# Kernel optimization log

Measured on AMD Instinct MI355X. Metric: run time of the kernel, lower is better.

## Reference

```python
import jax, jax.numpy as jnp
import numpy as np

EPS = 1e-10

def _cc_module(q, k, v):
    # q,k: [Bp, Cq, h, w]; v: [Bp, C, h, w]
    # cosine-normalize over channel dim (matches torch dim=-1 on (b,h,c) / dim=1 on (b,c,h))
    qn = q / (jnp.sqrt(jnp.sum(q * q, axis=1, keepdims=True)) + EPS)
    kn = k / (jnp.sqrt(jnp.sum(k * k, axis=1, keepdims=True)) + EPS)
    h = q.shape[2]
    energy_H = jnp.einsum('bchw,bcgw->bhwg', qn, kn)  # keys along column (height)
    energy_W = jnp.einsum('bchw,bchg->bhwg', qn, kn)  # keys along row (width)
    att = jax.nn.softmax(jnp.concatenate([energy_H, energy_W], axis=-1), axis=-1)
    att_H, att_W = att[..., :h], att[..., h:]
    out_H = jnp.einsum('bcgw,bhwg->bchw', v, att_H)
    out_W = jnp.einsum('bchg,bhwg->bchw', v, att_W)
    return out_H + out_W

def _grid_pa(q, k, v, nbin):
    # batch all bin*bin local patches of the grid into the leading dim
    B, C, H, W = v.shape
    ph, pw = H // nbin, W // nbin
    def split(t):
        c = t.shape[1]
        return t.reshape(B, c, nbin, ph, nbin, pw).transpose(0, 2, 4, 1, 3, 5).reshape(B * nbin * nbin, c, ph, pw)
    out = _cc_module(split(q), split(k), split(v))
    return out.reshape(B, nbin, nbin, C, ph, pw).transpose(0, 3, 1, 4, 2, 5).reshape(B, C, H, W)

def _conv1x1(x, w, b):
    return jnp.einsum('bchw,oc->bohw', x, w) + b[None, :, None, None]

def _cam(x, gamma):
    # channel attention: cosine similarity between channel vectors over spatial dim
    B, C, H, W = x.shape
    f = x.reshape(B, C, H * W)
    a = f / (jnp.sqrt(jnp.sum(f * f, axis=-1, keepdims=True)) + EPS)
    energy = jnp.einsum('bin,bjn->bij', a, a)  # [B, C, C]
    att = jax.nn.softmax(energy, axis=-1)
    out = jnp.einsum('bij,bjn->bin', att, f).reshape(B, C, H, W)
    return gamma * out + x

def setup_inputs() -> dict:
    key = jax.random.key(0)
    ks = jax.random.split(key, 8)
    B, C, H, W = 4, 512, 128, 128
    Cq = C // 4
    s = 0.05
    return {
        'x': jax.random.normal(ks[0], (B, C, H, W), jnp.float32),
        'w_q': jax.random.normal(ks[1], (Cq, C), jnp.float32) * s,
        'b_q': jnp.zeros((Cq,), jnp.float32),
        'w_k': jax.random.normal(ks[2], (Cq, C), jnp.float32) * s,
        'b_k': jnp.zeros((Cq,), jnp.float32),
        'w_v': jax.random.normal(ks[3], (C, C), jnp.float32) * s,
        'b_v': jnp.zeros((C,), jnp.float32),
        'gamma': jax.random.normal(ks[4], (1,), jnp.float32) * 0.1,
        'nbin': 4,
    }

def reference(x, w_q, b_q, w_k, b_k, w_v, b_v, gamma, nbin):
    # mode 'p_c_s': two rounds of grid criss-cross attention, then channel attention
    for _ in range(2):
        q = _conv1x1(x, w_q, b_q)
        k = _conv1x1(x, w_k, b_k)
        v = _conv1x1(x, w_v, b_v)
        x = _grid_pa(q, k, v, nbin)
    return _cam(x, gamma)
```

## Files before the change

kernel.cpp:

```cpp
#include <hip/hip_runtime.h>
#include <math.h>

constexpr int Bn = 4;
constexpr int Cc = 512;
constexpr int CQ = 128;
constexpr int Hh = 128, Ww = 128;
constexpr int Nn = Hh * Ww;
constexpr int NPATCH = 64;
constexpr float EPSf = 1e-10f;

typedef unsigned int u32;
typedef unsigned short u16;
typedef __attribute__((ext_vector_type(8))) short bf16x8;
typedef __attribute__((ext_vector_type(4))) float f32x4;

__device__ inline u16 f2bf(float f) {
    u32 u = __float_as_uint(f);
    u32 r = u + 0x7fffu + ((u >> 16) & 1u);
    return (u16)(r >> 16);
}
__device__ inline float bf2f(u16 h) { return __uint_as_float((u32)h << 16); }

#define GLOAD16(g, l) __builtin_amdgcn_global_load_lds( \
    (const __attribute__((address_space(1))) u32*)(g), \
    (__attribute__((address_space(3))) u32*)(l), 16, 0, 0)


__global__ __launch_bounds__(256) void conv_w(
    const float* __restrict__ wq, const float* __restrict__ bq,
    const float* __restrict__ wk, const float* __restrict__ bk,
    const float* __restrict__ wv, const float* __restrict__ bv,
    u16* __restrict__ wh, u16* __restrict__ wl, float* __restrict__ bcat)
{
    const int oc = blockIdx.x;
    const float* src; float bias;
    if (oc < 128)      { src = wq + (size_t)oc * 512;        bias = bq[oc]; }
    else if (oc < 256) { src = wk + (size_t)(oc-128) * 512;  bias = bk[oc-128]; }
    else               { src = wv + (size_t)(oc-256) * 512;  bias = bv[oc-256]; }
    for (int c = threadIdx.x; c < 512; c += 256) {
        float v = src[c];
        u16 h = f2bf(v);
        wh[(size_t)oc*512 + c] = h;
        wl[(size_t)oc*512 + c] = f2bf(v - bf2f(h));
    }
    if (threadIdx.x == 0) bcat[oc] = bias;
}

__global__ __launch_bounds__(256) void conv_x_t(
    const float* __restrict__ x, u16* __restrict__ xh, u16* __restrict__ xl)
{
    __shared__ float T[64][65];
    const int n0 = blockIdx.x * 64, c0 = blockIdx.y * 64, b = blockIdx.z;
    const int t = threadIdx.x;
    {
        const int cc = t >> 2, nn = (t & 3) * 16;
        const float* s = x + ((size_t)b*Cc + c0 + cc)*Nn + n0 + nn;
        #pragma unroll
        for (int u = 0; u < 16; u += 4) {
            float4 v = *(const float4*)(s + u);
            T[cc][nn+u]=v.x; T[cc][nn+u+1]=v.y; T[cc][nn+u+2]=v.z; T[cc][nn+u+3]=v.w;
        }
    }
    __syncthreads();
    {
        const int nn = t >> 2, cc0 = (t & 3) * 16;
        u16 hs[16] __attribute__((aligned(16)));
        u16 ls[16] __attribute__((aligned(16)));
        #pragma unroll
        for (int e = 0; e < 16; e++) {
            float v = T[cc0+e][nn];
            u16 h = f2bf(v);
            hs[e] = h; ls[e] = f2bf(v - bf2f(h));
        }
        const size_t o = ((size_t)b*Nn + n0 + nn)*Cc + c0 + cc0;
        *(uint4*)&xh[o]   = *(const uint4*)&hs[0];
        *(uint4*)&xh[o+8] = *(const uint4*)&hs[8];
        *(uint4*)&xl[o]   = *(const uint4*)&ls[0];
        *(uint4*)&xl[o+8] = *(const uint4*)&ls[8];
    }
}

__global__ __launch_bounds__(256) void conv_cl(
    const float* __restrict__ s, u16* __restrict__ h, u16* __restrict__ l, long n)
{
    const long i = (((long)blockIdx.x << 8) + threadIdx.x) << 3;
    if (i >= n) return;
    float4 a = *(const float4*)(s + i), b4 = *(const float4*)(s + i + 4);
    float v[8] = {a.x,a.y,a.z,a.w,b4.x,b4.y,b4.z,b4.w};
    u16 hs[8] __attribute__((aligned(16)));
    u16 ls[8] __attribute__((aligned(16)));
    #pragma unroll
    for (int e = 0; e < 8; e++) {
        u16 hh = f2bf(v[e]);
        hs[e] = hh; ls[e] = f2bf(v[e] - bf2f(hh));
    }
    *(uint4*)&h[i] = *(const uint4*)hs;
    *(uint4*)&l[i] = *(const uint4*)ls;
}

__global__ __launch_bounds__(256) void conv_t_cl(
    const float* __restrict__ x1, u16* __restrict__ th, u16* __restrict__ tl)
{
    __shared__ float T[64][65];
    const int n0 = blockIdx.x * 64, c0 = blockIdx.y * 64, b = blockIdx.z;
    const int t = threadIdx.x;
    {
        const int nn = t >> 2, cc0 = (t & 3) * 16;
        const float* s = x1 + ((size_t)b*Nn + n0 + nn)*Cc + c0 + cc0;
        #pragma unroll
        for (int u = 0; u < 16; u += 4) {
            float4 v = *(const float4*)(s + u);
            T[nn][cc0+u]=v.x; T[nn][cc0+u+1]=v.y; T[nn][cc0+u+2]=v.z; T[nn][cc0+u+3]=v.w;
        }
    }
    __syncthreads();
    {
        const int cc = t >> 2, nn0 = (t & 3) * 16;
        u16 hs[16] __attribute__((aligned(16)));
        u16 ls[16] __attribute__((aligned(16)));
        #pragma unroll
        for (int e = 0; e < 16; e++) {
            float v = T[nn0+e][cc];
            u16 h = f2bf(v);
            hs[e] = h; ls[e] = f2bf(v - bf2f(h));
        }
        const size_t o = ((size_t)b*Cc + c0 + cc)*Nn + n0 + nn0;
        *(uint4*)&th[o]   = *(const uint4*)&hs[0];
        *(uint4*)&th[o+8] = *(const uint4*)&hs[8];
        *(uint4*)&tl[o]   = *(const uint4*)&ls[0];
        *(uint4*)&tl[o+8] = *(const uint4*)&ls[8];
    }
}


__global__ __launch_bounds__(256) void qkv_mfma(
    const u16* __restrict__ xh, const u16* __restrict__ xl,
    const u16* __restrict__ wh, const u16* __restrict__ wl,
    const float* __restrict__ bcat,
    float* __restrict__ q_t, float* __restrict__ k_t, float* __restrict__ v_t)
{
    __shared__ char Ash[16384];
    __shared__ char Bsh[16384];
    const int t = threadIdx.x, lane = t & 63, wid = t >> 6;
    const int n0 = blockIdx.x * 128, oc0 = blockIdx.y * 128, b = blockIdx.z;
    const size_t bN = (size_t)b * Nn;

    float* outp; int ocb, OC;
    if (oc0 == 0)        { outp = q_t; ocb = 0;         OC = CQ; }
    else if (oc0 == 128) { outp = k_t; ocb = 0;         OC = CQ; }
    else                 { outp = v_t; ocb = oc0 - 256; OC = Cc; }

    const u16* sA[4]; const u16* sB[4];
    #pragma unroll
    for (int q = 0; q < 4; q++) {
        const int p = ((wid*4 + q) << 10) + lane*16;
        const int row = p >> 7;
        const int lchunk = ((p >> 4) & 7) ^ (row & 7);
        const int ko = (lchunk & 3) * 8;
        sA[q] = ((lchunk < 4) ? xh : xl) + (bN + n0 + row)*(size_t)Cc + ko;
        sB[q] = ((lchunk < 4) ? wh : wl) + (size_t)(oc0 + row)*Cc + ko;
    }

    const int wr = wid >> 1, wc = wid & 1;
    int aoff[4], boff[4];
    #pragma unroll
    for (int m = 0; m < 4; m++) {
        const int ra = (wr << 6) + (m << 4) + (lane & 15);
        aoff[m] = (ra << 7) + ((((lane >> 4) << 4)) ^ ((ra & 7) << 4));
        const int rb = (wc << 6) + (m << 4) + (lane & 15);
        boff[m] = (rb << 7) + ((((lane >> 4) << 4)) ^ ((rb & 7) << 4));
    }

    f32x4 acc[4][4];
    #pragma unroll
    for (int m = 0; m < 4; m++)
        #pragma unroll
        for (int n = 0; n < 4; n++) acc[m][n] = (f32x4){0.f, 0.f, 0.f, 0.f};

    for (int ks = 0; ks < 16; ks++) {
        if (ks) __syncthreads();
        #pragma unroll
        for (int q = 0; q < 4; q++) {
            GLOAD16(sA[q], Ash + ((wid*4 + q) << 10));
            GLOAD16(sB[q], Bsh + ((wid*4 + q) << 10));
            sA[q] += 32; sB[q] += 32;
        }
        __syncthreads();
        bf16x8 ah[4], al[4], bh[4], bl[4];
        #pragma unroll
        for (int m = 0; m < 4; m++) {
            ah[m] = *(const bf16x8*)(Ash + aoff[m]);
            al[m] = *(const bf16x8*)(Ash + (aoff[m] ^ 64));
            bh[m] = *(const bf16x8*)(Bsh + boff[m]);
            bl[m] = *(const bf16x8*)(Bsh + (boff[m] ^ 64));
        }
        #pragma unroll
        for (int m = 0; m < 4; m++)
            #pragma unroll
            for (int n = 0; n < 4; n++) {
                acc[m][n] = __builtin_amdgcn_mfma_f32_16x16x32_bf16(ah[m], bh[n], acc[m][n], 0, 0, 0);
                acc[m][n] = __builtin_amdgcn_mfma_f32_16x16x32_bf16(ah[m], bl[n], acc[m][n], 0, 0, 0);
                acc[m][n] = __builtin_amdgcn_mfma_f32_16x16x32_bf16(al[m], bh[n], acc[m][n], 0, 0, 0);
            }
    }

    const int col = lane & 15, rq = lane >> 4;
    #pragma unroll
    for (int n = 0; n < 4; n++) {
        const int oc = (wc << 6) + (n << 4) + col;
        const float bias = bcat[oc0 + oc];
        #pragma unroll
        for (int m = 0; m < 4; m++) {
            #pragma unroll
            for (int r = 0; r < 4; r++) {
                const int nrow = n0 + (wr << 6) + (m << 4) + (rq << 2) + r;
                outp[(bN + nrow)*OC + ocb + oc] = acc[m][n][r] + bias;
            }
        }
    }
}

__global__ __launch_bounds__(256) void gram_mfma(
    const u16* __restrict__ fTh, const u16* __restrict__ fTl,
    float* __restrict__ Gp)
{
    __shared__ char Ash[16384];
    __shared__ char Bsh[16384];
    const int t = threadIdx.x, lane = t & 63, wid = t >> 6;
    const int i0 = blockIdx.x * 128, j0 = blockIdx.y * 128;
    const int b = blockIdx.z >> 3, kc = blockIdx.z & 7;
    const size_t cb = (size_t)b * 512 * Nn;

    const u16* sA[4]; const u16* sB[4];
    #pragma unroll
    for (int q = 0; q < 4; q++) {
        const int p = ((wid*4 + q) << 10) + lane*16;
        const int row = p >> 7;
        const int lchunk = ((p >> 4) & 7) ^ (row & 7);
        const int ko = (lchunk & 3) * 8;
        const u16* s = (lchunk < 4) ? fTh : fTl;
        sA[q] = s + cb + (size_t)(i0 + row)*Nn + kc*2048 + ko;
        sB[q] = s + cb + (size_t)(j0 + row)*Nn + kc*2048 + ko;
    }

    const int wr = wid >> 1, wc = wid & 1;
    int aoff[4], boff[4];
    #pragma unroll
    for (int m = 0; m < 4; m++) {
        const int ra = (wr << 6) + (m << 4) + (lane & 15);
        aoff[m] = (ra << 7) + ((((lane >> 4) << 4)) ^ ((ra & 7) << 4));
        const int rb = (wc << 6) + (m << 4) + (lane & 15);
        boff[m] = (rb << 7) + ((((lane >> 4) << 4)) ^ ((rb & 7) << 4));
    }

    f32x4 acc[4][4];
    #pragma unroll
    for (int m = 0; m < 4; m++)
        #pragma unroll
        for (int n = 0; n < 4; n++) acc[m][n] = (f32x4){0.f, 0.f, 0.f, 0.f};

    for (int ks = 0; ks < 64; ks++) {
        if (ks) __syncthreads();
        #pragma unroll
        for (int q = 0; q < 4; q++) {
            GLOAD16(sA[q], Ash + ((wid*4 + q) << 10));
            GLOAD16(sB[q], Bsh + ((wid*4 + q) << 10));
            sA[q] += 32; sB[q] += 32;
        }
        __syncthreads();
        bf16x8 ah[4], al[4], bh[4], bl[4];
        #pragma unroll
        for (int m = 0; m < 4; m++) {
            ah[m] = *(const bf16x8*)(Ash + aoff[m]);
            al[m] = *(const bf16x8*)(Ash + (aoff[m] ^ 64));
            bh[m] = *(const bf16x8*)(Bsh + boff[m]);
            bl[m] = *(const bf16x8*)(Bsh + (boff[m] ^ 64));
        }
        #pragma unroll
        for (int m = 0; m < 4; m++)
            #pragma unroll
            for (int n = 0; n < 4; n++) {
                acc[m][n] = __builtin_amdgcn_mfma_f32_16x16x32_bf16(ah[m], bh[n], acc[m][n], 0, 0, 0);
                acc[m][n] = __builtin_amdgcn_mfma_f32_16x16x32_bf16(ah[m], bl[n], acc[m][n], 0, 0, 0);
                acc[m][n] = __builtin_amdgcn_mfma_f32_16x16x32_bf16(al[m], bh[n], acc[m][n], 0, 0, 0);
            }
    }

    float* gp = Gp + (size_t)(kc*4 + b) * 512 * 512;
    const int col = lane & 15, rq = lane >> 4;
    #pragma unroll
    for (int m = 0; m < 4; m++)
        #pragma unroll
        for (int r = 0; r < 4; r++) {
            const int ri = i0 + (wr << 6) + (m << 4) + (rq << 2) + r;
            #pragma unroll
            for (int n = 0; n < 4; n++)
                gp[(size_t)ri*512 + j0 + (wc << 6) + (n << 4) + col] = acc[m][n][r];
        }
}

__global__ __launch_bounds__(256) void camout_mfma(
    const u16* __restrict__ Ph, const u16* __restrict__ Pl,
    const u16* __restrict__ x1h, const u16* __restrict__ x1l,
    const u16* __restrict__ fTh, const u16* __restrict__ fTl,
    const float* __restrict__ gamma, float* __restrict__ out)
{
    __shared__ char Ash[16384];
    __shared__ char Bsh[16384];
    const int t = threadIdx.x, lane = t & 63, wid = t >> 6;
    const int n0 = blockIdx.x * 128, i0 = blockIdx.y * 128, b = blockIdx.z;
    const size_t bN = (size_t)b * Nn;

    const u16* sA[4]; const u16* sB[4];
    #pragma unroll
    for (int q = 0; q < 4; q++) {
        const int p = ((wid*4 + q) << 10) + lane*16;
        const int row = p >> 7;
        const int lchunk = ((p >> 4) & 7) ^ (row & 7);
        const int ko = (lchunk & 3) * 8;
        sA[q] = ((lchunk < 4) ? Ph : Pl) + ((size_t)b*512 + i0 + row)*512 + ko;
        sB[q] = ((lchunk < 4) ? x1h : x1l) + (bN + n0 + row)*(size_t)Cc + ko;
    }

    const int wr = wid >> 1, wc = wid & 1;
    int aoff[4], boff[4];
    #pragma unroll
    for (int m = 0; m < 4; m++) {
        const int ra = (wr << 6) + (m << 4) + (lane & 15);
        aoff[m] = (ra << 7) + ((((lane >> 4) << 4)) ^ ((ra & 7) << 4));
        const int rb = (wc << 6) + (m << 4) + (lane & 15);
        boff[m] = (rb << 7) + ((((lane >> 4) << 4)) ^ ((rb & 7) << 4));
    }

    f32x4 acc[4][4];
    #pragma unroll
    for (int m = 0; m < 4; m++)
        #pragma unroll
        for (int n = 0; n < 4; n++) acc[m][n] = (f32x4){0.f, 0.f, 0.f, 0.f};

    for (int ks = 0; ks < 16; ks++) {
        if (ks) __syncthreads();
        #pragma unroll
        for (int q = 0; q < 4; q++) {
            GLOAD16(sA[q], Ash + ((wid*4 + q) << 10));
            GLOAD16(sB[q], Bsh + ((wid*4 + q) << 10));
            sA[q] += 32; sB[q] += 32;
        }
        __syncthreads();
        bf16x8 ah[4], al[4], bh[4], bl[4];
        #pragma unroll
        for (int m = 0; m < 4; m++) {
            ah[m] = *(const bf16x8*)(Ash + aoff[m]);
            al[m] = *(const bf16x8*)(Ash + (aoff[m] ^ 64));
            bh[m] = *(const bf16x8*)(Bsh + boff[m]);
            bl[m] = *(const bf16x8*)(Bsh + (boff[m] ^ 64));
        }
        #pragma unroll
        for (int m = 0; m < 4; m++)
            #pragma unroll
            for (int n = 0; n < 4; n++) {
                acc[m][n] = __builtin_amdgcn_mfma_f32_16x16x32_bf16(ah[m], bh[n], acc[m][n], 0, 0, 0);
                acc[m][n] = __builtin_amdgcn_mfma_f32_16x16x32_bf16(ah[m], bl[n], acc[m][n], 0, 0, 0);
                acc[m][n] = __builtin_amdgcn_mfma_f32_16x16x32_bf16(al[m], bh[n], acc[m][n], 0, 0, 0);
            }
    }

    const float gm = gamma[0];
    const int col = lane & 15, rq = lane >> 4;
    #pragma unroll
    for (int m = 0; m < 4; m++)
        #pragma unroll
        for (int r = 0; r < 4; r++) {
            const int i = i0 + (wr << 6) + (m << 4) + (rq << 2) + r;
            const size_t rb = ((size_t)b*512 + i)*Nn;
            #pragma unroll
            for (int n = 0; n < 4; n++) {
                const int nn = n0 + (wc << 6) + (n << 4) + col;
                const float res = bf2f(fTh[rb + nn]) + bf2f(fTl[rb + nn]);
                out[rb + nn] = fmaf(gm, acc[m][n][r], res);
            }
        }
}

__global__ __launch_bounds__(256) void qk_norms(
    const float* __restrict__ q_t, const float* __restrict__ k_t,
    float* __restrict__ nq, float* __restrict__ nk)
{
    const int pos = blockIdx.x * 256 + threadIdx.x;
    const float* qp = q_t + (size_t)pos * CQ;
    const float* kp = k_t + (size_t)pos * CQ;
    float sq = 0.f, sk = 0.f;
    #pragma unroll
    for (int c = 0; c < CQ; c += 4) {
        float4 a = *(const float4*)&qp[c];
        float4 bb = *(const float4*)&kp[c];
        sq += a.x*a.x + a.y*a.y + a.z*a.z + a.w*a.w;
        sk += bb.x*bb.x + bb.y*bb.y + bb.z*bb.z + bb.w*bb.w;
    }
    nq[pos] = sqrtf(sq) + EPSf;
    nk[pos] = sqrtf(sk) + EPSf;
}

__global__ __launch_bounds__(256) void energy_H(
    const float* __restrict__ q_t, const float* __restrict__ k_t,
    const float* __restrict__ nq, const float* __restrict__ nk,
    float* __restrict__ att)
{
    __shared__ float Qs[32][129], Ks[32][129];
    __shared__ float nqs[32], nks[32];
    const int w = blockIdx.x, p = blockIdx.y;
    const int b = p >> 4, pi = (p >> 2) & 3, pj = p & 3;
    const int gw = pj*32 + w;
    const int t = threadIdx.x;
    {
        const int h  = t >> 3;
        const int c0 = (t & 7) * 16;
        const size_t base = ((size_t)b*Nn + (size_t)(pi*32 + h)*Ww + gw) * CQ + c0;
        #pragma unroll
        for (int u = 0; u < 16; u += 4) {
            float4 qa = *(const float4*)&q_t[base + u];
            float4 ka = *(const float4*)&k_t[base + u];
            Qs[h][c0+u]=qa.x; Qs[h][c0+u+1]=qa.y; Qs[h][c0+u+2]=qa.z; Qs[h][c0+u+3]=qa.w;
            Ks[h][c0+u]=ka.x; Ks[h][c0+u+1]=ka.y; Ks[h][c0+u+2]=ka.z; Ks[h][c0+u+3]=ka.w;
        }
    }
    if (t < 32) {
        const size_t pp = (size_t)b*Nn + (size_t)(pi*32 + t)*Ww + gw;
        nqs[t] = nq[pp]; nks[t] = nk[pp];
    }
    __syncthreads();
    const int h0 = (t & 15) * 2, g0 = (t >> 4) * 2;
    float a00=0,a01=0,a10=0,a11=0;
    #pragma unroll 4
    for (int c = 0; c < CQ; c++) {
        float q0 = Qs[h0][c], q1 = Qs[h0+1][c];
        float k0 = Ks[g0][c], k1 = Ks[g0+1][c];
        a00 = fmaf(q0,k0,a00); a01 = fmaf(q0,k1,a01);
        a10 = fmaf(q1,k0,a10); a11 = fmaf(q1,k1,a11);
    }
    const size_t ab = (((size_t)p*32 + h0)*32 + w)*64;
    att[ab + g0]            = a00 / (nqs[h0]   * nks[g0]);
    att[ab + g0 + 1]        = a01 / (nqs[h0]   * nks[g0+1]);
    att[ab + 2048 + g0]     = a10 / (nqs[h0+1] * nks[g0]);
    att[ab + 2048 + g0 + 1] = a11 / (nqs[h0+1] * nks[g0+1]);
}

__global__ __launch_bounds__(256) void energy_W(
    const float* __restrict__ q_t, const float* __restrict__ k_t,
    const float* __restrict__ nq, const float* __restrict__ nk,
    float* __restrict__ att)
{
    __shared__ float Qs[32][129], Ks[32][129];
    __shared__ float nqs[32], nks[32];
    const int h = blockIdx.x, p = blockIdx.y;
    const int b = p >> 4, pi = (p >> 2) & 3, pj = p & 3;
    const int gh = pi*32 + h;
    const size_t rowpos = (size_t)b*Nn + (size_t)gh*Ww + pj*32;
    const int t = threadIdx.x;
    {
        const int wl = t >> 3;
        const int c0 = (t & 7) * 16;
        const size_t base = (rowpos + wl) * CQ + c0;
        #pragma unroll
        for (int u = 0; u < 16; u += 4) {
            float4 qa = *(const float4*)&q_t[base + u];
            float4 ka = *(const float4*)&k_t[base + u];
            Qs[wl][c0+u]=qa.x; Qs[wl][c0+u+1]=qa.y; Qs[wl][c0+u+2]=qa.z; Qs[wl][c0+u+3]=qa.w;
            Ks[wl][c0+u]=ka.x; Ks[wl][c0+u+1]=ka.y; Ks[wl][c0+u+2]=ka.z; Ks[wl][c0+u+3]=ka.w;
        }
    }
    if (t < 32) { nqs[t] = nq[rowpos + t]; nks[t] = nk[rowpos + t]; }
    __syncthreads();
    const int w0 = (t & 15) * 2, g0 = (t >> 4) * 2;
    float a00=0,a01=0,a10=0,a11=0;
    #pragma unroll 4
    for (int c = 0; c < CQ; c++) {
        float q0 = Qs[w0][c], q1 = Qs[w0+1][c];
        float k0 = Ks[g0][c], k1 = Ks[g0+1][c];
        a00 = fmaf(q0,k0,a00); a01 = fmaf(q0,k1,a01);
        a10 = fmaf(q1,k0,a10); a11 = fmaf(q1,k1,a11);
    }
    const size_t ab = (((size_t)p*32 + h)*32 + w0)*64 + 32;
    att[ab + g0]          = a00 / (nqs[w0]   * nks[g0]);
    att[ab + g0 + 1]      = a01 / (nqs[w0]   * nks[g0+1]);
    att[ab + 64 + g0]     = a10 / (nqs[w0+1] * nks[g0]);
    att[ab + 64 + g0 + 1] = a11 / (nqs[w0+1] * nks[g0+1]);
}

__global__ __launch_bounds__(256) void softmax64(float* __restrict__ att)
{
    const size_t idx = (size_t)blockIdx.x * 256 + threadIdx.x;
    float* row = att + idx * 64;
    float v[64];
    float m = -1e30f;
    #pragma unroll
    for (int i = 0; i < 64; i += 4) {
        float4 x4 = *(const float4*)&row[i];
        v[i]=x4.x; v[i+1]=x4.y; v[i+2]=x4.z; v[i+3]=x4.w;
        m = fmaxf(m, fmaxf(fmaxf(x4.x,x4.y), fmaxf(x4.z,x4.w)));
    }
    float s = 0.f;
    #pragma unroll
    for (int i = 0; i < 64; i++) { v[i] = __expf(v[i] - m); s += v[i]; }
    const float inv = 1.f / s;
    #pragma unroll
    for (int i = 0; i < 64; i += 4) {
        float4 x4 = {v[i]*inv, v[i+1]*inv, v[i+2]*inv, v[i+3]*inv};
        *(float4*)&row[i] = x4;
    }
}

__global__ __launch_bounds__(256) void cc_outH(
    const float* __restrict__ v_t, const float* __restrict__ att,
    float* __restrict__ x1)
{
    __shared__ float Vs[32][256];
    __shared__ float At[32][33];
    const int w = blockIdx.x, p = blockIdx.y;
    const int b = p >> 4, pi = (p >> 2) & 3, pj = p & 3;
    const int gw = pj*32 + w;
    const int t = threadIdx.x;
    {
        const int hh = t >> 3, g0 = (t & 7) * 4;
        const float* arow = att + (((size_t)p*32 + hh)*32 + w)*64 + g0;
        float4 a = *(const float4*)arow;
        At[g0][hh]=a.x; At[g0+1][hh]=a.y; At[g0+2][hh]=a.z; At[g0+3][hh]=a.w;
    }
    const int s  = t & 63, hg = t >> 6;
    const int cl = s * 4, h0 = hg * 8;
    for (int half = 0; half < 2; half++) {
        __syncthreads();
        {
            const int g = t >> 3, c0 = (t & 7) * 32;
            const float* src = v_t + ((size_t)b*Nn + (size_t)(pi*32 + g)*Ww + gw)*Cc + half*256 + c0;
            #pragma unroll
            for (int u = 0; u < 32; u += 4)
                *(float4*)&Vs[g][c0+u] = *(const float4*)&src[u];
        }
        __syncthreads();
        float acc[8][4];
        #pragma unroll
        for (int i = 0; i < 8; i++) { acc[i][0]=0.f; acc[i][1]=0.f; acc[i][2]=0.f; acc[i][3]=0.f; }
        #pragma unroll 4
        for (int g = 0; g < 32; g++) {
            const float4 va = *(const float4*)&Vs[g][cl];
            #pragma unroll
            for (int hh = 0; hh < 8; hh++) {
                const float a = At[g][h0+hh];
                acc[hh][0] = fmaf(va.x, a, acc[hh][0]);
                acc[hh][1] = fmaf(va.y, a, acc[hh][1]);
                acc[hh][2] = fmaf(va.z, a, acc[hh][2]);
                acc[hh][3] = fmaf(va.w, a, acc[hh][3]);
            }
        }
        #pragma unroll
        for (int hh = 0; hh < 8; hh++) {
            float4 o = {acc[hh][0], acc[hh][1], acc[hh][2], acc[hh][3]};
            *(float4*)&x1[((size_t)b*Nn + (size_t)(pi*32 + h0+hh)*Ww + gw)*Cc + half*256 + cl] = o;
        }
    }
}

__global__ __launch_bounds__(256) void cc_outW(
    const float* __restrict__ v_t, const float* __restrict__ att,
    float* __restrict__ x1)
{
    __shared__ float Vs[32][256];
    __shared__ float At[32][33];
    const int h = blockIdx.x, p = blockIdx.y;
    const int b = p >> 4, pi = (p >> 2) & 3, pj = p & 3;
    const int gh = pi*32 + h;
    const size_t rowpos = (size_t)b*Nn + (size_t)gh*Ww + pj*32;
    const int t = threadIdx.x;
    {
        const int wl = t >> 3, g0 = (t & 7) * 4;
        const float* arow = att + (((size_t)p*32 + h)*32 + wl)*64 + 32 + g0;
        float4 a = *(const float4*)arow;
        At[g0][wl]=a.x; At[g0+1][wl]=a.y; At[g0+2][wl]=a.z; At[g0+3][wl]=a.w;
    }
    const int s  = t & 63, wg = t >> 6;
    const int cl = s * 4, w0 = wg * 8;
    for (int half = 0; half < 2; half++) {
        __syncthreads();
        {
            const int g = t >> 3, c0 = (t & 7) * 32;
            const float* src = v_t + (rowpos + g)*Cc + half*256 + c0;
            #pragma unroll
            for (int u = 0; u < 32; u += 4)
                *(float4*)&Vs[g][c0+u] = *(const float4*)&src[u];
        }
        __syncthreads();
        float acc[8][4];
        #pragma unroll
        for (int i = 0; i < 8; i++) { acc[i][0]=0.f; acc[i][1]=0.f; acc[i][2]=0.f; acc[i][3]=0.f; }
        #pragma unroll 4
        for (int g = 0; g < 32; g++) {
            const float4 va = *(const float4*)&Vs[g][cl];
            #pragma unroll
            for (int ww = 0; ww < 8; ww++) {
                const float a = At[g][w0+ww];
                acc[ww][0] = fmaf(va.x, a, acc[ww][0]);
                acc[ww][1] = fmaf(va.y, a, acc[ww][1]);
                acc[ww][2] = fmaf(va.z, a, acc[ww][2]);
                acc[ww][3] = fmaf(va.w, a, acc[ww][3]);
            }
        }
        #pragma unroll
        for (int ww = 0; ww < 8; ww++) {
            float* op = x1 + (rowpos + w0+ww)*Cc + half*256 + cl;
            float4 r = *(const float4*)op;
            r.x += acc[ww][0]; r.y += acc[ww][1]; r.z += acc[ww][2]; r.w += acc[ww][3];
            *(float4*)op = r;
        }
    }
}

__global__ void zero_kernel(float* __restrict__ p, int n)
{
    const int i = blockIdx.x * 256 + threadIdx.x;
    if (i < n) p[i] = 0.f;
}

__global__ __launch_bounds__(256) void cam_normacc(
    const float* __restrict__ x1, float* __restrict__ nf2)
{
    const int b = blockIdx.x >> 6, ch = blockIdx.x & 63;
    const int t = threadIdx.x;
    const float* base = x1 + ((size_t)b*Nn + (size_t)ch*256)*Cc;
    float s0 = 0.f, s1 = 0.f;
    #pragma unroll 8
    for (int r = 0; r < 256; r++) {
        const float v0 = base[(size_t)r*Cc + t];
        const float v1 = base[(size_t)r*Cc + t + 256];
        s0 = fmaf(v0, v0, s0);
        s1 = fmaf(v1, v1, s1);
    }
    atomicAdd(&nf2[b*Cc + t],       s0);
    atomicAdd(&nf2[b*Cc + t + 256], s1);
}

__global__ __launch_bounds__(256) void cam_softmax(
    const float* __restrict__ Gp, const float* __restrict__ nf2,
    float* __restrict__ P)
{
    const int b = blockIdx.x >> 9, i = blockIdx.x & 511;
    const int t = threadIdx.x;
    __shared__ float red[8];
    const size_t roff = ((size_t)b*512 + i) * 512;
    float v0 = 0.f, v1 = 0.f;
    #pragma unroll
    for (int kc = 0; kc < 8; kc++) {
        const float* gp = Gp + (size_t)(kc*4 + b)*512*512 + (size_t)i*512;
        v0 += gp[t];
        v1 += gp[t + 256];
    }
    const float nfi = sqrtf(nf2[b*512 + i]) + EPSf;
    const float nj0 = sqrtf(nf2[b*512 + t]) + EPSf;
    const float nj1 = sqrtf(nf2[b*512 + t + 256]) + EPSf;
    float e0 = v0 / (nfi*nj0), e1 = v1 / (nfi*nj1);
    float m = fmaxf(e0, e1);
    #pragma unroll
    for (int o = 32; o > 0; o >>= 1) m = fmaxf(m, __shfl_xor(m, o, 64));
    if ((t & 63) == 0) red[t >> 6] = m;
    __syncthreads();
    m = fmaxf(fmaxf(red[0], red[1]), fmaxf(red[2], red[3]));
    float p0 = __expf(e0 - m), p1 = __expf(e1 - m);
    float s = p0 + p1;
    #pragma unroll
    for (int o = 32; o > 0; o >>= 1) s += __shfl_xor(s, o, 64);
    if ((t & 63) == 0) red[4 + (t >> 6)] = s;
    __syncthreads();
    s = red[4] + red[5] + red[6] + red[7];
    const float inv = 1.f / s;
    P[roff + t]       = p0 * inv;
    P[roff + t + 256] = p1 * inv;
}

extern "C" void kernel_launch(void* const* d_in, const int* in_sizes, int n_in,
                              void* d_out, int out_size, void* d_ws, size_t ws_size,
                              hipStream_t stream)
{
    (void)in_sizes; (void)n_in; (void)out_size; (void)ws_size;
    const float* x    = (const float*)d_in[0];
    const float* wqp  = (const float*)d_in[1];
    const float* bqp  = (const float*)d_in[2];
    const float* wkp  = (const float*)d_in[3];
    const float* bkp  = (const float*)d_in[4];
    const float* wvp  = (const float*)d_in[5];
    const float* bvp  = (const float*)d_in[6];
    const float* gmp  = (const float*)d_in[7];
    float* out = (float*)d_out;

    char* W = (char*)d_ws;
    float* q_t = (float*)(W);
    float* k_t = (float*)(W + 33554432);
    float* v_t = (float*)(W + 67108864);
    float* x1  = (float*)(W + 201326592);
    float* att = (float*)(W + 335544320);
    float* nq  = (float*)(W + 352321536);
    float* nk  = (float*)(W + 352583680);
    u16*   xh  = (u16*)  (W + 352845824);
    u16*   xl  = (u16*)  (W + 419954688);
    u16*   wh  = (u16*)  (W + 487063552);
    u16*   wl  = (u16*)  (W + 487849984);
    float* bcat= (float*)(W + 488636416);
    float* nf2 = q_t;
    float* Gp  = (float*)(W + 16384);
    float* P   = (float*)(W + 16384 + 33554432);
    u16*   Ph  = (u16*)  (W + 16384 + 33554432 + 4194304);
    u16*   Pl  = (u16*)  (W + 16384 + 33554432 + 4194304 + 2097152);
    u16*   fTh = (u16*)(W + 67108864);
    u16*   fTl = (u16*)(W + 67108864 + 67108864);

    conv_w  <<<dim3(768),      256, 0, stream>>>(wqp,bqp, wkp,bkp, wvp,bvp, wh, wl, bcat);
    conv_x_t<<<dim3(256,8,4),  256, 0, stream>>>(x, xh, xl);

    for (int it = 0; it < 2; it++) {
        if (it == 1)
            conv_cl<<<dim3(16384), 256, 0, stream>>>(x1, xh, xl, (long)Bn*Nn*Cc);
        qkv_mfma <<<dim3(128,6,4), 256, 0, stream>>>(xh, xl, wh, wl, bcat, q_t, k_t, v_t);
        qk_norms <<<dim3(256),     256, 0, stream>>>(q_t, k_t, nq, nk);
        energy_H <<<dim3(32,64),   256, 0, stream>>>(q_t, k_t, nq, nk, att);
        energy_W <<<dim3(32,64),   256, 0, stream>>>(q_t, k_t, nq, nk, att);
        softmax64<<<dim3(256),     256, 0, stream>>>(att);
        cc_outH  <<<dim3(32,64),   256, 0, stream>>>(v_t, att, x1);
        cc_outW  <<<dim3(32,64),   256, 0, stream>>>(v_t, att, x1);
    }

    conv_cl   <<<dim3(16384),   256, 0, stream>>>(x1, xh, xl, (long)Bn*Nn*Cc);
    conv_t_cl <<<dim3(256,8,4), 256, 0, stream>>>(x1, fTh, fTl);
    zero_kernel<<<dim3(8),      256, 0, stream>>>(nf2, 2048);
    cam_normacc<<<dim3(256),    256, 0, stream>>>(x1, nf2);
    gram_mfma <<<dim3(4,4,32),  256, 0, stream>>>(fTh, fTl, Gp);
    cam_softmax<<<dim3(2048),   256, 0, stream>>>(Gp, nf2, P);
    conv_cl   <<<dim3(512),     256, 0, stream>>>(P, Ph, Pl, (long)Bn*512*512);
    camout_mfma<<<dim3(128,4,4),256, 0, stream>>>(Ph, Pl, xh, xl, fTh, fTl, gmp, out);
}
```

Measured before the change: 1.468 ms.

## Fuse bf16 hi/lo split into attention outputs and norms into energy kernels

The criss-cross output kernels now write x1 directly as bf16 hi/lo pairs, so the separate fp32 x1 buffer and the conv_cl split passes go away. The q/k norms are computed inside the energy kernels, which removes the qk_norms kernel. The CAM channel norms are read from the transposed hi/lo buffer with one block per channel and no atomics, which also drops the zero kernel. This removes several launches and full-tensor fp32 passes, but cc_outW now does a read-modify-write with a re-split into hi/lo, which adds a little rounding.

```diff
diff --git a/kernel.cpp b/kernel.cpp
--- a/kernel.cpp
+++ b/kernel.cpp
@@ -99,19 +99,19 @@
 }
 
 __global__ __launch_bounds__(256) void conv_t_cl(
-    const float* __restrict__ x1, u16* __restrict__ th, u16* __restrict__ tl)
-{
-    __shared__ float T[64][65];
+    const u16* __restrict__ x1h, const u16* __restrict__ x1l,
+    u16* __restrict__ th, u16* __restrict__ tl)
+{
+    __shared__ u16 Th[64][72], Tl[64][72];
     const int n0 = blockIdx.x * 64, c0 = blockIdx.y * 64, b = blockIdx.z;
     const int t = threadIdx.x;
     {
         const int nn = t >> 2, cc0 = (t & 3) * 16;
-        const float* s = x1 + ((size_t)b*Nn + n0 + nn)*Cc + c0 + cc0;
-        #pragma unroll
-        for (int u = 0; u < 16; u += 4) {
-            float4 v = *(const float4*)(s + u);
-            T[nn][cc0+u]=v.x; T[nn][cc0+u+1]=v.y; T[nn][cc0+u+2]=v.z; T[nn][cc0+u+3]=v.w;
-        }
+        const size_t src = ((size_t)b*Nn + n0 + nn)*Cc + c0 + cc0;
+        *(uint4*)&Th[nn][cc0]     = *(const uint4*)&x1h[src];
+        *(uint4*)&Th[nn][cc0 + 8] = *(const uint4*)&x1h[src + 8];
+        *(uint4*)&Tl[nn][cc0]     = *(const uint4*)&x1l[src];
+        *(uint4*)&Tl[nn][cc0 + 8] = *(const uint4*)&x1l[src + 8];
     }
     __syncthreads();
     {
@@ -119,11 +119,7 @@
         u16 hs[16] __attribute__((aligned(16)));
         u16 ls[16] __attribute__((aligned(16)));
         #pragma unroll
-        for (int e = 0; e < 16; e++) {
-            float v = T[nn0+e][cc];
-            u16 h = f2bf(v);
-            hs[e] = h; ls[e] = f2bf(v - bf2f(h));
-        }
+        for (int e = 0; e < 16; e++) { hs[e] = Th[nn0+e][cc]; ls[e] = Tl[nn0+e][cc]; }
         const size_t o = ((size_t)b*Cc + c0 + cc)*Nn + n0 + nn0;
         *(uint4*)&th[o]   = *(const uint4*)&hs[0];
         *(uint4*)&th[o+8] = *(const uint4*)&hs[8];
@@ -382,31 +378,12 @@
         }
 }
 
-__global__ __launch_bounds__(256) void qk_norms(
-    const float* __restrict__ q_t, const float* __restrict__ k_t,
-    float* __restrict__ nq, float* __restrict__ nk)
-{
-    const int pos = blockIdx.x * 256 + threadIdx.x;
-    const float* qp = q_t + (size_t)pos * CQ;
-    const float* kp = k_t + (size_t)pos * CQ;
-    float sq = 0.f, sk = 0.f;
-    #pragma unroll
-    for (int c = 0; c < CQ; c += 4) {
-        float4 a = *(const float4*)&qp[c];
-        float4 bb = *(const float4*)&kp[c];
-        sq += a.x*a.x + a.y*a.y + a.z*a.z + a.w*a.w;
-        sk += bb.x*bb.x + bb.y*bb.y + bb.z*bb.z + bb.w*bb.w;
-    }
-    nq[pos] = sqrtf(sq) + EPSf;
-    nk[pos] = sqrtf(sk) + EPSf;
-}
-
 __global__ __launch_bounds__(256) void energy_H(
     const float* __restrict__ q_t, const float* __restrict__ k_t,
-    const float* __restrict__ nq, const float* __restrict__ nk,
     float* __restrict__ att)
 {
     __shared__ float Qs[32][129], Ks[32][129];
+    __shared__ float pq[32][8], pk[32][8];
     __shared__ float nqs[32], nks[32];
     const int w = blockIdx.x, p = blockIdx.y;
     const int b = p >> 4, pi = (p >> 2) & 3, pj = p & 3;
@@ -416,17 +393,24 @@
         const int h  = t >> 3;
         const int c0 = (t & 7) * 16;
         const size_t base = ((size_t)b*Nn + (size_t)(pi*32 + h)*Ww + gw) * CQ + c0;
+        float sq = 0.f, sk = 0.f;
         #pragma unroll
         for (int u = 0; u < 16; u += 4) {
             float4 qa = *(const float4*)&q_t[base + u];
             float4 ka = *(const float4*)&k_t[base + u];
             Qs[h][c0+u]=qa.x; Qs[h][c0+u+1]=qa.y; Qs[h][c0+u+2]=qa.z; Qs[h][c0+u+3]=qa.w;
             Ks[h][c0+u]=ka.x; Ks[h][c0+u+1]=ka.y; Ks[h][c0+u+2]=ka.z; Ks[h][c0+u+3]=ka.w;
-        }
-    }
+            sq += qa.x*qa.x + qa.y*qa.y + qa.z*qa.z + qa.w*qa.w;
+            sk += ka.x*ka.x + ka.y*ka.y + ka.z*ka.z + ka.w*ka.w;
+        }
+        pq[h][t & 7] = sq; pk[h][t & 7] = sk;
+    }
+    __syncthreads();
     if (t < 32) {
-        const size_t pp = (size_t)b*Nn + (size_t)(pi*32 + t)*Ww + gw;
-        nqs[t] = nq[pp]; nks[t] = nk[pp];
+        float s1 = 0.f, s2 = 0.f;
+        #pragma unroll
+        for (int j = 0; j < 8; j++) { s1 += pq[t][j]; s2 += pk[t][j]; }
+        nqs[t] = sqrtf(s1) + EPSf; nks[t] = sqrtf(s2) + EPSf;
     }
     __syncthreads();
     const int h0 = (t & 15) * 2, g0 = (t >> 4) * 2;
@@ -447,10 +431,10 @@
 
 __global__ __launch_bounds__(256) void energy_W(
     const float* __restrict__ q_t, const float* __restrict__ k_t,
-    const float* __restrict__ nq, const float* __restrict__ nk,
     float* __restrict__ att)
 {
     __shared__ float Qs[32][129], Ks[32][129];
+    __shared__ float pq[32][8], pk[32][8];
     __shared__ float nqs[32], nks[32];
     const int h = blockIdx.x, p = blockIdx.y;
     const int b = p >> 4, pi = (p >> 2) & 3, pj = p & 3;
@@ -461,15 +445,25 @@
         const int wl = t >> 3;
         const int c0 = (t & 7) * 16;
         const size_t base = (rowpos + wl) * CQ + c0;
+        float sq = 0.f, sk = 0.f;
         #pragma unroll
         for (int u = 0; u < 16; u += 4) {
             float4 qa = *(const float4*)&q_t[base + u];
             float4 ka = *(const float4*)&k_t[base + u];
             Qs[wl][c0+u]=qa.x; Qs[wl][c0+u+1]=qa.y; Qs[wl][c0+u+2]=qa.z; Qs[wl][c0+u+3]=qa.w;
             Ks[wl][c0+u]=ka.x; Ks[wl][c0+u+1]=ka.y; Ks[wl][c0+u+2]=ka.z; Ks[wl][c0+u+3]=ka.w;
-        }
-    }
-    if (t < 32) { nqs[t] = nq[rowpos + t]; nks[t] = nk[rowpos + t]; }
+            sq += qa.x*qa.x + qa.y*qa.y + qa.z*qa.z + qa.w*qa.w;
+            sk += ka.x*ka.x + ka.y*ka.y + ka.z*ka.z + ka.w*ka.w;
+        }
+        pq[wl][t & 7] = sq; pk[wl][t & 7] = sk;
+    }
+    __syncthreads();
+    if (t < 32) {
+        float s1 = 0.f, s2 = 0.f;
+        #pragma unroll
+        for (int j = 0; j < 8; j++) { s1 += pq[t][j]; s2 += pk[t][j]; }
+        nqs[t] = sqrtf(s1) + EPSf; nks[t] = sqrtf(s2) + EPSf;
+    }
     __syncthreads();
     const int w0 = (t & 15) * 2, g0 = (t >> 4) * 2;
     float a00=0,a01=0,a10=0,a11=0;
@@ -512,7 +506,7 @@
 
 __global__ __launch_bounds__(256) void cc_outH(
     const float* __restrict__ v_t, const float* __restrict__ att,
-    float* __restrict__ x1)
+    u16* __restrict__ x1h, u16* __restrict__ x1l)
 {
     __shared__ float Vs[32][256];
     __shared__ float At[32][33];
@@ -555,15 +549,24 @@
         }
         #pragma unroll
         for (int hh = 0; hh < 8; hh++) {
-            float4 o = {acc[hh][0], acc[hh][1], acc[hh][2], acc[hh][3]};
-            *(float4*)&x1[((size_t)b*Nn + (size_t)(pi*32 + h0+hh)*Ww + gw)*Cc + half*256 + cl] = o;
+            u16 hs[4] __attribute__((aligned(8)));
+            u16 ls[4] __attribute__((aligned(8)));
+            #pragma unroll
+            for (int j = 0; j < 4; j++) {
+                const float v = acc[hh][j];
+                const u16 h2 = f2bf(v);
+                hs[j] = h2; ls[j] = f2bf(v - bf2f(h2));
+            }
+            const size_t o = ((size_t)b*Nn + (size_t)(pi*32 + h0+hh)*Ww + gw)*Cc + half*256 + cl;
+            *(uint2*)&x1h[o] = *(const uint2*)hs;
+            *(uint2*)&x1l[o] = *(const uint2*)ls;
         }
     }
 }
 
 __global__ __launch_bounds__(256) void cc_outW(
     const float* __restrict__ v_t, const float* __restrict__ att,
-    float* __restrict__ x1)
+    u16* __restrict__ x1h, u16* __restrict__ x1l)
 {
     __shared__ float Vs[32][256];
     __shared__ float At[32][33];
@@ -607,36 +610,55 @@
         }
         #pragma unroll
         for (int ww = 0; ww < 8; ww++) {
-            float* op = x1 + (rowpos + w0+ww)*Cc + half*256 + cl;
-            float4 r = *(const float4*)op;
-            r.x += acc[ww][0]; r.y += acc[ww][1]; r.z += acc[ww][2]; r.w += acc[ww][3];
-            *(float4*)op = r;
-        }
-    }
-}
-
-__global__ void zero_kernel(float* __restrict__ p, int n)
-{
-    const int i = blockIdx.x * 256 + threadIdx.x;
-    if (i < n) p[i] = 0.f;
+            const size_t o = (rowpos + w0+ww)*Cc + half*256 + cl;
+            const uint2 ph = *(const uint2*)&x1h[o];
+            const uint2 pl = *(const uint2*)&x1l[o];
+            float v[4];
+            v[0] = bf2f((u16)ph.x)        + bf2f((u16)pl.x)        + acc[ww][0];
+            v[1] = bf2f((u16)(ph.x>>16))  + bf2f((u16)(pl.x>>16))  + acc[ww][1];
+            v[2] = bf2f((u16)ph.y)        + bf2f((u16)pl.y)        + acc[ww][2];
+            v[3] = bf2f((u16)(ph.y>>16))  + bf2f((u16)(pl.y>>16))  + acc[ww][3];
+            u16 hs[4] __attribute__((aligned(8)));
+            u16 ls[4] __attribute__((aligned(8)));
+            #pragma unroll
+            for (int j = 0; j < 4; j++) {
+                const u16 h2 = f2bf(v[j]);
+                hs[j] = h2; ls[j] = f2bf(v[j] - bf2f(h2));
+            }
+            *(uint2*)&x1h[o] = *(const uint2*)hs;
+            *(uint2*)&x1l[o] = *(const uint2*)ls;
+        }
+    }
 }
 
 __global__ __launch_bounds__(256) void cam_normacc(
-    const float* __restrict__ x1, float* __restrict__ nf2)
-{
-    const int b = blockIdx.x >> 6, ch = blockIdx.x & 63;
+    const u16* __restrict__ fTh, const u16* __restrict__ fTl, float* __restrict__ nf2)
+{
+    const int bc = blockIdx.x;
+    const u16* ph = fTh + (size_t)bc * Nn;
+    const u16* pl = fTl + (size_t)bc * Nn;
     const int t = threadIdx.x;
-    const float* base = x1 + ((size_t)b*Nn + (size_t)ch*256)*Cc;
-    float s0 = 0.f, s1 = 0.f;
-    #pragma unroll 8
-    for (int r = 0; r < 256; r++) {
-        const float v0 = base[(size_t)r*Cc + t];
-        const float v1 = base[(size_t)r*Cc + t + 256];
-        s0 = fmaf(v0, v0, s0);
-        s1 = fmaf(v1, v1, s1);
-    }
-    atomicAdd(&nf2[b*Cc + t],       s0);
-    atomicAdd(&nf2[b*Cc + t + 256], s1);
+    float s = 0.f;
+    #pragma unroll
+    for (int base = 0; base < Nn; base += 2048) {
+        const int i = base + t*8;
+        const uint4 hv = *(const uint4*)&ph[i];
+        const uint4 lv = *(const uint4*)&pl[i];
+        const u32 hw[4] = {hv.x, hv.y, hv.z, hv.w};
+        const u32 lw[4] = {lv.x, lv.y, lv.z, lv.w};
+        #pragma unroll
+        for (int j = 0; j < 4; j++) {
+            const float a  = bf2f((u16)hw[j])       + bf2f((u16)lw[j]);
+            const float b2 = bf2f((u16)(hw[j]>>16)) + bf2f((u16)(lw[j]>>16));
+            s = fmaf(a, a, s); s = fmaf(b2, b2, s);
+        }
+    }
+    #pragma unroll
+    for (int o = 32; o > 0; o >>= 1) s += __shfl_xor(s, o, 64);
+    __shared__ float red[4];
+    if ((t & 63) == 0) red[t >> 6] = s;
+    __syncthreads();
+    if (t == 0) nf2[bc] = red[0] + red[1] + red[2] + red[3];
 }
 
 __global__ __launch_bounds__(256) void cam_softmax(
@@ -695,44 +717,40 @@
     float* q_t = (float*)(W);
     float* k_t = (float*)(W + 33554432);
     float* v_t = (float*)(W + 67108864);
-    float* x1  = (float*)(W + 201326592);
+    u16*   x1h = (u16*)  (W + 201326592);
+    u16*   x1l = (u16*)  (W + 268435456);
     float* att = (float*)(W + 335544320);
-    float* nq  = (float*)(W + 352321536);
-    float* nk  = (float*)(W + 352583680);
-    u16*   xh  = (u16*)  (W + 352845824);
-    u16*   xl  = (u16*)  (W + 419954688);
-    u16*   wh  = (u16*)  (W + 487063552);
-    u16*   wl  = (u16*)  (W + 487849984);
-    float* bcat= (float*)(W + 488636416);
-    float* nf2 = q_t;
+    u16*   xh  = (u16*)  (W + 352321536);
+    u16*   xl  = (u16*)  (W + 419430400);
+    u16*   wh  = (u16*)  (W + 486539264);
+    u16*   wl  = (u16*)  (W + 487325696);
+    float* bcat= (float*)(W + 488112128);
+    float* nf2 = (float*)(W);
     float* Gp  = (float*)(W + 16384);
     float* P   = (float*)(W + 16384 + 33554432);
     u16*   Ph  = (u16*)  (W + 16384 + 33554432 + 4194304);
     u16*   Pl  = (u16*)  (W + 16384 + 33554432 + 4194304 + 2097152);
     u16*   fTh = (u16*)(W + 67108864);
-    u16*   fTl = (u16*)(W + 67108864 + 67108864);
+    u16*   fTl = (u16*)(W + 134217728);
 
     conv_w  <<<dim3(768),      256, 0, stream>>>(wqp,bqp, wkp,bkp, wvp,bvp, wh, wl, bcat);
     conv_x_t<<<dim3(256,8,4),  256, 0, stream>>>(x, xh, xl);
 
     for (int it = 0; it < 2; it++) {
-        if (it == 1)
-            conv_cl<<<dim3(16384), 256, 0, stream>>>(x1, xh, xl, (long)Bn*Nn*Cc);
-        qkv_mfma <<<dim3(128,6,4), 256, 0, stream>>>(xh, xl, wh, wl, bcat, q_t, k_t, v_t);
-        qk_norms <<<dim3(256),     256, 0, stream>>>(q_t, k_t, nq, nk);
-        energy_H <<<dim3(32,64),   256, 0, stream>>>(q_t, k_t, nq, nk, att);
-        energy_W <<<dim3(32,64),   256, 0, stream>>>(q_t, k_t, nq, nk, att);
+        const u16* ah = (it == 0) ? xh : x1h;
+        const u16* al = (it == 0) ? xl : x1l;
+        qkv_mfma <<<dim3(128,6,4), 256, 0, stream>>>(ah, al, wh, wl, bcat, q_t, k_t, v_t);
+        energy_H <<<dim3(32,64),   256, 0, stream>>>(q_t, k_t, att);
+        energy_W <<<dim3(32,64),   256, 0, stream>>>(q_t, k_t, att);
         softmax64<<<dim3(256),     256, 0, stream>>>(att);
-        cc_outH  <<<dim3(32,64),   256, 0, stream>>>(v_t, att, x1);
-        cc_outW  <<<dim3(32,64),   256, 0, stream>>>(v_t, att, x1);
-    }
-
-    conv_cl   <<<dim3(16384),   256, 0, stream>>>(x1, xh, xl, (long)Bn*Nn*Cc);
-    conv_t_cl <<<dim3(256,8,4), 256, 0, stream>>>(x1, fTh, fTl);
-    zero_kernel<<<dim3(8),      256, 0, stream>>>(nf2, 2048);
-    cam_normacc<<<dim3(256),    256, 0, stream>>>(x1, nf2);
-    gram_mfma <<<dim3(4,4,32),  256, 0, stream>>>(fTh, fTl, Gp);
-    cam_softmax<<<dim3(2048),   256, 0, stream>>>(Gp, nf2, P);
-    conv_cl   <<<dim3(512),     256, 0, stream>>>(P, Ph, Pl, (long)Bn*512*512);
-    camout_mfma<<<dim3(128,4,4),256, 0, stream>>>(Ph, Pl, xh, xl, fTh, fTl, gmp, out);
-}
+        cc_outH  <<<dim3(32,64),   256, 0, stream>>>(v_t, att, x1h, x1l);
+        cc_outW  <<<dim3(32,64),   256, 0, stream>>>(v_t, att, x1h, x1l);
+    }
+
+    conv_t_cl  <<<dim3(256,8,4), 256, 0, stream>>>(x1h, x1l, fTh, fTl);
+    cam_normacc<<<dim3(2048),    256, 0, stream>>>(fTh, fTl, nf2);
+    gram_mfma  <<<dim3(4,4,32),  256, 0, stream>>>(fTh, fTl, Gp);
+    cam_softmax<<<dim3(2048),    256, 0, stream>>>(Gp, nf2, P);
+    conv_cl    <<<dim3(512),     256, 0, stream>>>(P, Ph, Pl, (long)Bn*512*512);
+    camout_mfma<<<dim3(128,4,4), 256, 0, stream>>>(Ph, Pl, x1h, x1l, fTh, fTl, gmp, out);
+}
```

Measured after the change: 1.374 ms. 6.4% less time.
